# Performance work log

Measured on AMD Instinct MI355X. Metric: run time of the kernel, lower is better.

Reference implementation:

```python
import jax, jax.numpy as jnp
import numpy as np

OUT, IN = 4096, 4096
BITS = 4
B, S = 4, 2048


def setup_inputs() -> dict:
    key = jax.random.key(0)
    k1, k2, k3, k4, k5, k6 = jax.random.split(key, 6)
    x = jax.random.normal(k1, (B, S, IN), dtype=jnp.float32)
    indices = jax.random.randint(k2, (OUT, IN), 0, 2 ** BITS, dtype=jnp.int32)
    centroids = jax.random.normal(k3, (2 ** BITS,), dtype=jnp.float32)
    # Pi stands in for the seeded rotation matrix (orthogonality not required for math check)
    Pi = jax.random.normal(k4, (IN, IN), dtype=jnp.float32) / np.sqrt(IN)
    row_norms = jax.random.uniform(k5, (OUT,), dtype=jnp.float32) + 0.5
    bias = jax.random.normal(k6, (OUT,), dtype=jnp.float32)
    return {"x": x, "indices": indices, "centroids": centroids, "Pi": Pi,
            "row_norms": row_norms, "bias": bias}


def reference(x, indices, centroids, Pi, row_norms, bias):
    # Dequantize: centroid gather -> inverse rotation -> per-row rescale
    y_hat = centroids[indices]                    # (out, in)
    W = (y_hat @ Pi) * row_norms[:, None]         # (out, in)
    # F.linear: x @ W^T + b
    return jnp.einsum('bsi,oi->bso', x, W) + bias
```

## Files before the change

kernel.cpp:

```cpp
#include <hip/hip_runtime.h>
#include <hip/hip_bf16.h>

typedef unsigned short u16;
typedef __bf16 bf16x8 __attribute__((ext_vector_type(8)));
typedef float f32x4 __attribute__((ext_vector_type(4)));


__device__ __forceinline__ u16 f32_to_bf16(float f) {
    unsigned int u = __float_as_uint(f);
    unsigned int r = (u + 0x7FFFu + ((u >> 16) & 1u)) >> 16;
    return (u16)r;
}

__device__ __forceinline__ unsigned pack2(float a, float b) {
    return (unsigned)f32_to_bf16(a) | ((unsigned)f32_to_bf16(b) << 16);
}

__device__ __forceinline__ void load_lds16(const void* g, void* s) {
    __builtin_amdgcn_global_load_lds(
        (__attribute__((address_space(1))) void*)g,
        (__attribute__((address_space(3))) void*)s,
        16, 0, 0);
}


__global__ __launch_bounds__(256) void convert_f32_bf16(
        const float* __restrict__ in, u16* __restrict__ out) {
    int i = blockIdx.x * 256 + threadIdx.x;
    const float4* in4 = (const float4*)in;
    float4 v0 = in4[(size_t)i * 2];
    float4 v1 = in4[(size_t)i * 2 + 1];
    uint4 r;
    r.x = pack2(v0.x, v0.y);
    r.y = pack2(v0.z, v0.w);
    r.z = pack2(v1.x, v1.y);
    r.w = pack2(v1.z, v1.w);
    ((uint4*)out)[i] = r;
}


__global__ __launch_bounds__(256) void dequant_kernel(
        const int* __restrict__ idx, const float* __restrict__ cent,
        u16* __restrict__ out) {
    __shared__ float lut[16];
    if (threadIdx.x < 16) lut[threadIdx.x] = cent[threadIdx.x];
    __syncthreads();
    int i = blockIdx.x * 256 + threadIdx.x;
    const int4* in4 = (const int4*)idx;
    int4 a = in4[(size_t)i * 2];
    int4 b = in4[(size_t)i * 2 + 1];
    uint4 r;
    r.x = pack2(lut[a.x], lut[a.y]);
    r.y = pack2(lut[a.z], lut[a.w]);
    r.z = pack2(lut[b.x], lut[b.y]);
    r.w = pack2(lut[b.z], lut[b.w]);
    ((uint4*)out)[i] = r;
}


__global__ __launch_bounds__(256) void transpose_to_bf16(
        const float* __restrict__ Pi, u16* __restrict__ PiT) {
    __shared__ float tile[32][33];
    const int tx = threadIdx.x;
    const int ty = threadIdx.y;
    const int j0 = blockIdx.x * 32;
    const int k0 = blockIdx.y * 32;
#pragma unroll
    for (int i = 0; i < 4; i++)
        tile[ty + 8 * i][tx] = Pi[(size_t)(k0 + ty + 8 * i) * 4096 + j0 + tx];
    __syncthreads();
#pragma unroll
    for (int i = 0; i < 4; i++)
        PiT[(size_t)(j0 + ty + 8 * i) * 4096 + k0 + tx] =
            f32_to_bf16(tile[tx][ty + 8 * i]);
}


template <int MODE>
__global__ __launch_bounds__(512, 2) void gemm_bt(
        const u16* __restrict__ A, const u16* __restrict__ Bm,
        const float* __restrict__ aux, float* __restrict__ Cf,
        u16* __restrict__ Cb, int M, int N, int K) {
    __shared__ u16 As[4 * 8192];
    __shared__ u16 Bs[4 * 8192];

    const int tid  = threadIdx.x;
    const int lane = tid & 63;
    const int wv   = tid >> 6;
    const int wr   = wv >> 2;
    const int wc   = wv & 3;

    const int nwg  = gridDim.x * gridDim.y;
    const int orig = blockIdx.y * gridDim.x + blockIdx.x;
    const int swz  = (orig & 7) * (nwg >> 3) + (orig >> 3);
    const int m0   = (swz >> 4) << 8;
    const int n0   = (swz & 15) << 8;

    const int sr  = tid >> 2;
    const int csw = ((tid & 3) ^ ((tid >> 3) & 3)) << 3;
    const u16* a0 = A  + (size_t)(m0 + sr) * K + csw;
    const u16* a1 = A  + (size_t)(m0 + 128 + sr) * K + csw;
    const u16* b0 = Bm + (size_t)(n0 + sr) * K + csw;
    const u16* b1 = Bm + (size_t)(n0 + 128 + sr) * K + csw;
    u16* dA = As + tid * 8;
    u16* dB = Bs + tid * 8;

    const int l15   = lane & 15;
    const int ck    = (((lane >> 4) ^ ((lane >> 1) & 3)) << 3);
    const int laneA = (wr * 128 + l15) * 32 + ck;
    const int laneB = (wc * 64 + l15) * 32 + ck;

    f32x4 acc[8][4];
#pragma unroll
    for (int i = 0; i < 8; i++)
#pragma unroll
        for (int j = 0; j < 4; j++) acc[i][j] = (f32x4){0.f, 0.f, 0.f, 0.f};
    bf16x8 bF[4];

#define STAGE_A(SLOT, COL) do { \
        load_lds16(a0 + (COL), dA + (SLOT) * 8192); \
        load_lds16(a1 + (COL), dA + (SLOT) * 8192 + 4096); } while (0)
#define STAGE_B(SLOT, COL) do { \
        load_lds16(b0 + (COL), dB + (SLOT) * 8192); \
        load_lds16(b1 + (COL), dB + (SLOT) * 8192 + 4096); } while (0)
#define VM(N) asm volatile("s_waitcnt vmcnt(" #N ")" ::: "memory")

#define PHASE(SB, MH, RB, STAGE, WAIT) do { \
        bf16x8 aF[4]; \
        _Pragma("unroll") \
        for (int i_ = 0; i_ < 4; i_++) \
            aF[i_] = *(const bf16x8*)&As[(SB) + laneA + ((MH) * 4 + i_) * 512]; \
        if (RB) { \
            _Pragma("unroll") \
            for (int i_ = 0; i_ < 4; i_++) \
                bF[i_] = *(const bf16x8*)&Bs[(SB) + laneB + i_ * 512]; \
        } \
        STAGE; \
        WAIT; \
        __builtin_amdgcn_s_barrier(); \
        asm volatile("s_waitcnt lgkmcnt(0)" ::: "memory"); \
        __builtin_amdgcn_sched_barrier(0); \
        __builtin_amdgcn_s_setprio(1); \
        _Pragma("unroll") \
        for (int i_ = 0; i_ < 4; i_++) { \
            _Pragma("unroll") \
            for (int n_ = 0; n_ < 4; n_++) \
                acc[(MH) * 4 + i_][n_] = __builtin_amdgcn_mfma_f32_16x16x32_bf16( \
                    aF[i_], bF[n_], acc[(MH) * 4 + i_][n_], 0, 0, 0); \
        } \
        __builtin_amdgcn_s_setprio(0); \
        __builtin_amdgcn_s_barrier(); \
    } while (0)

    const int NT = K >> 6;

    STAGE_A(0, 0);
    STAGE_B(0, 0);
    STAGE_A(1, 32);
    STAGE_B(1, 32);
    STAGE_A(2, 64);
    VM(6);
    __builtin_amdgcn_s_barrier();

#pragma unroll 1
    for (int t = 0; t < NT - 2; t += 2) {
        const int c1 = (t + 1) * 64;
        const int c2 = c1 + 64;
        PHASE(0,     0, 1, STAGE_B(2, c1),      ((void)0));
        PHASE(0,     1, 0, STAGE_A(3, c1 + 32), VM(6));
        PHASE(8192,  0, 1, STAGE_B(3, c1 + 32), ((void)0));
        PHASE(8192,  1, 0, STAGE_A(0, c2),      VM(6));
        PHASE(16384, 0, 1, STAGE_B(0, c2),      ((void)0));
        PHASE(16384, 1, 0, STAGE_A(1, c2 + 32), VM(6));
        PHASE(24576, 0, 1, STAGE_B(1, c2 + 32), ((void)0));
        PHASE(24576, 1, 0, STAGE_A(2, c2 + 64), VM(6));
    }

    {
        const int cT = (NT - 1) * 64;
        PHASE(0,    0, 1, STAGE_B(2, cT),      ((void)0));
        PHASE(0,    1, 0, STAGE_A(3, cT + 32), VM(6));
        PHASE(8192, 0, 1, STAGE_B(3, cT + 32), ((void)0));
        PHASE(8192, 1, 0, ((void)0),           VM(4));
    }
    {
        PHASE(16384, 0, 1, ((void)0), ((void)0));
        PHASE(16384, 1, 0, ((void)0), VM(0));
        PHASE(24576, 0, 1, ((void)0), ((void)0));
        PHASE(24576, 1, 0, ((void)0), ((void)0));
    }

#undef PHASE
#undef VM
#undef STAGE_B
#undef STAGE_A

    const int colf = l15;
    const int r0   = (lane >> 4) << 2;
#pragma unroll
    for (int m = 0; m < 8; m++) {
        const int row = m0 + wr * 128 + m * 16 + r0;
#pragma unroll
        for (int n = 0; n < 4; n++) {
            const int col = n0 + wc * 64 + n * 16 + colf;
            if (MODE == 0) {
#pragma unroll
                for (int e = 0; e < 4; e++)
                    Cb[(size_t)(row + e) * N + col] =
                        f32_to_bf16(acc[m][n][e] * aux[row + e]);
            } else {
                const float bv = aux[col];
#pragma unroll
                for (int e = 0; e < 4; e++)
                    Cf[(size_t)(row + e) * N + col] = acc[m][n][e] + bv;
            }
        }
    }
}


extern "C" void kernel_launch(void* const* d_in, const int* in_sizes, int n_in,
                              void* d_out, int out_size, void* d_ws, size_t ws_size,
                              hipStream_t stream) {
    const float* x         = (const float*)d_in[0];
    const int*   indices   = (const int*)d_in[1];
    const float* centroids = (const float*)d_in[2];
    const float* Pi        = (const float*)d_in[3];
    const float* row_norms = (const float*)d_in[4];
    const float* bias      = (const float*)d_in[5];
    float* out = (float*)d_out;

    u16* x_bf = (u16*)d_ws;
    u16* y_bf = x_bf + (size_t)33554432;
    u16* pi_t = y_bf + (size_t)16777216;
    u16* w_bf = pi_t + (size_t)16777216;

    convert_f32_bf16<<<16384, 256, 0, stream>>>(x, x_bf);
    dequant_kernel<<<8192, 256, 0, stream>>>(indices, centroids, y_bf);
    transpose_to_bf16<<<dim3(128, 128), dim3(32, 8), 0, stream>>>(Pi, pi_t);
    gemm_bt<0><<<dim3(16, 16), 512, 0, stream>>>(
        y_bf, pi_t, row_norms, nullptr, w_bf, 4096, 4096, 4096);
    gemm_bt<1><<<dim3(16, 32), 512, 0, stream>>>(
        x_bf, w_bf, bias, out, nullptr, 8192, 4096, 4096);
}
```

Baseline: 718.6 us.

## Software-pipeline LDS fragment reads behind MFMA in bf16 GEMM main loop

Restructures the GEMM main loop so each section issues its MFMAs on fragments already in registers, then reads the next fragments from LDS and issues the next global->LDS stage. One barrier per section replaces two, and the sched_barrier is removed. The prologue now pre-stages three full slots. The tail is folded into the loop, with dummy loads from column 0 on the last iterations. This is meant to hide LDS read latency behind matrix math and cut sync overhead. It risks WAR hazards on LDS slots and wasted redundant loads at the end.

```diff
diff --git a/kernel.cpp b/kernel.cpp
--- a/kernel.cpp
+++ b/kernel.cpp
@@ -115,7 +115,7 @@
     for (int i = 0; i < 8; i++)
 #pragma unroll
         for (int j = 0; j < 4; j++) acc[i][j] = (f32x4){0.f, 0.f, 0.f, 0.f};
-    bf16x8 bF[4];
+    bf16x8 aF[4], bF[4];
 
 #define STAGE_A(SLOT, COL) do { \
         load_lds16(a0 + (COL), dA + (SLOT) * 8192); \
@@ -123,75 +123,63 @@
 #define STAGE_B(SLOT, COL) do { \
         load_lds16(b0 + (COL), dB + (SLOT) * 8192); \
         load_lds16(b1 + (COL), dB + (SLOT) * 8192 + 4096); } while (0)
-#define VM(N) asm volatile("s_waitcnt vmcnt(" #N ")" ::: "memory")
-
-#define PHASE(SB, MH, RB, STAGE, WAIT) do { \
-        bf16x8 aF[4]; \
-        _Pragma("unroll") \
-        for (int i_ = 0; i_ < 4; i_++) \
-            aF[i_] = *(const bf16x8*)&As[(SB) + laneA + ((MH) * 4 + i_) * 512]; \
-        if (RB) { \
-            _Pragma("unroll") \
-            for (int i_ = 0; i_ < 4; i_++) \
-                bF[i_] = *(const bf16x8*)&Bs[(SB) + laneB + i_ * 512]; \
-        } \
-        STAGE; \
-        WAIT; \
+#define VMW(N) asm volatile("s_waitcnt vmcnt(" #N ")" ::: "memory")
+
+#define SECTION(MHC, STG, RSB, RMH, RDB, VMS) do { \
         __builtin_amdgcn_s_barrier(); \
         asm volatile("s_waitcnt lgkmcnt(0)" ::: "memory"); \
-        __builtin_amdgcn_sched_barrier(0); \
+        STG; \
         __builtin_amdgcn_s_setprio(1); \
         _Pragma("unroll") \
         for (int i_ = 0; i_ < 4; i_++) { \
             _Pragma("unroll") \
             for (int n_ = 0; n_ < 4; n_++) \
-                acc[(MH) * 4 + i_][n_] = __builtin_amdgcn_mfma_f32_16x16x32_bf16( \
-                    aF[i_], bF[n_], acc[(MH) * 4 + i_][n_], 0, 0, 0); \
+                acc[(MHC) * 4 + i_][n_] = __builtin_amdgcn_mfma_f32_16x16x32_bf16( \
+                    aF[i_], bF[n_], acc[(MHC) * 4 + i_][n_], 0, 0, 0); \
         } \
         __builtin_amdgcn_s_setprio(0); \
-        __builtin_amdgcn_s_barrier(); \
+        _Pragma("unroll") \
+        for (int i_ = 0; i_ < 4; i_++) \
+            aF[i_] = *(const bf16x8*)&As[(RSB) + laneA + ((RMH) * 4 + i_) * 512]; \
+        if (RDB) { \
+            _Pragma("unroll") \
+            for (int i_ = 0; i_ < 4; i_++) \
+                bF[i_] = *(const bf16x8*)&Bs[(RSB) + laneB + i_ * 512]; \
+        } \
+        VMS; \
     } while (0)
 
     const int NT = K >> 6;
 
-    STAGE_A(0, 0);
-    STAGE_B(0, 0);
-    STAGE_A(1, 32);
-    STAGE_B(1, 32);
-    STAGE_A(2, 64);
-    VM(6);
+    STAGE_A(0, 0);  STAGE_B(0, 0);
+    STAGE_A(1, 32); STAGE_B(1, 32);
+    STAGE_A(2, 64); STAGE_B(2, 64);
+    VMW(8);
     __builtin_amdgcn_s_barrier();
+#pragma unroll
+    for (int i_ = 0; i_ < 4; i_++)
+        aF[i_] = *(const bf16x8*)&As[laneA + i_ * 512];
+#pragma unroll
+    for (int i_ = 0; i_ < 4; i_++)
+        bF[i_] = *(const bf16x8*)&Bs[laneB + i_ * 512];
 
 #pragma unroll 1
-    for (int t = 0; t < NT - 2; t += 2) {
-        const int c1 = (t + 1) * 64;
-        const int c2 = c1 + 64;
-        PHASE(0,     0, 1, STAGE_B(2, c1),      ((void)0));
-        PHASE(0,     1, 0, STAGE_A(3, c1 + 32), VM(6));
-        PHASE(8192,  0, 1, STAGE_B(3, c1 + 32), ((void)0));
-        PHASE(8192,  1, 0, STAGE_A(0, c2),      VM(6));
-        PHASE(16384, 0, 1, STAGE_B(0, c2),      ((void)0));
-        PHASE(16384, 1, 0, STAGE_A(1, c2 + 32), VM(6));
-        PHASE(24576, 0, 1, STAGE_B(1, c2 + 32), ((void)0));
-        PHASE(24576, 1, 0, STAGE_A(2, c2 + 64), VM(6));
+    for (int t = 0; t < NT; t += 2) {
+        const int cB1 = (t + 1) * 64 + 32;
+        const int c2  = (t + 2 < NT) ? (t + 2) * 64 : 0;
+        const int c3  = (t + 3 < NT) ? (t + 3) * 64 : 0;
+        SECTION(0, STAGE_A(3, cB1),     0,     1, 0, VMW(6));
+        SECTION(1, STAGE_B(3, cB1),     8192,  0, 1, (void)0);
+        SECTION(0, STAGE_A(0, c2),      8192,  1, 0, VMW(6));
+        SECTION(1, STAGE_B(0, c2),      16384, 0, 1, (void)0);
+        SECTION(0, STAGE_A(1, c2 + 32), 16384, 1, 0, VMW(6));
+        SECTION(1, STAGE_B(1, c2 + 32), 24576, 0, 1, (void)0);
+        SECTION(0, STAGE_A(2, c3),      24576, 1, 0, VMW(6));
+        SECTION(1, STAGE_B(2, c3),      0,     0, 1, (void)0);
     }
 
-    {
-        const int cT = (NT - 1) * 64;
-        PHASE(0,    0, 1, STAGE_B(2, cT),      ((void)0));
-        PHASE(0,    1, 0, STAGE_A(3, cT + 32), VM(6));
-        PHASE(8192, 0, 1, STAGE_B(3, cT + 32), ((void)0));
-        PHASE(8192, 1, 0, ((void)0),           VM(4));
-    }
-    {
-        PHASE(16384, 0, 1, ((void)0), ((void)0));
-        PHASE(16384, 1, 0, ((void)0), VM(0));
-        PHASE(24576, 0, 1, ((void)0), ((void)0));
-        PHASE(24576, 1, 0, ((void)0), ((void)0));
-    }
-
-#undef PHASE
-#undef VM
+#undef SECTION
+#undef VMW
 #undef STAGE_B
 #undef STAGE_A
 
```

Measured after the change: 677.7 us. 1.06x faster.
